# Performance work log

Measured on AMD Instinct MI355X. Metric: run time of the kernel, lower is better.

## Reference

```python
import jax, jax.numpy as jnp
import numpy as np

N_NODES = 100_000
N_EDGES_RAND = 800_000
N_GRAPHS = 2048
IN_FEATS = 74        # CanonicalAtomFeaturizer size
HEADS = 4            # dgllife GAT default num_heads
OUT_FEATS = 32       # dgllife GAT default hidden_feats=[32,32]
PRED_DIM = 128
NEG_SLOPE = 0.2      # dgllife default alpha


def setup_inputs() -> dict:
    key = jax.random.key(0)
    ks = jax.random.split(key, 16)
    feats = jax.random.normal(ks[0], (N_NODES, IN_FEATS), jnp.float32)
    src_r = jax.random.randint(ks[1], (N_EDGES_RAND,), 0, N_NODES, dtype=jnp.int32)
    dst_r = jax.random.randint(ks[2], (N_EDGES_RAND,), 0, N_NODES, dtype=jnp.int32)
    loops = jnp.arange(N_NODES, dtype=jnp.int32)  # self-loops -> no zero in-degree
    src = jnp.concatenate([src_r, loops])
    dst = jnp.concatenate([dst_r, loops])
    # sorted, every graph non-empty, ~49 nodes per molecule
    graph_ids = ((jnp.arange(N_NODES, dtype=jnp.int64) * N_GRAPHS) // N_NODES).astype(jnp.int32)

    def lin(k, i, o):
        return (jax.random.normal(k, (i, o), jnp.float32) / np.sqrt(i)).astype(jnp.float32)

    HF = HEADS * OUT_FEATS
    return {
        'feats': feats, 'src': src, 'dst': dst, 'graph_ids': graph_ids,
        'fc1_w': lin(ks[3], IN_FEATS, HF),
        'attn_l1': jax.random.normal(ks[4], (HEADS, OUT_FEATS), jnp.float32) * 0.1,
        'attn_r1': jax.random.normal(ks[5], (HEADS, OUT_FEATS), jnp.float32) * 0.1,
        'res1_w': lin(ks[6], IN_FEATS, HF),   # residual proj (in != heads*out)
        'bias1': jnp.zeros((HF,), jnp.float32),
        'fc2_w': lin(ks[7], HF, HF),
        'attn_l2': jax.random.normal(ks[8], (HEADS, OUT_FEATS), jnp.float32) * 0.1,
        'attn_r2': jax.random.normal(ks[9], (HEADS, OUT_FEATS), jnp.float32) * 0.1,
        'bias2': jnp.zeros((HF,), jnp.float32),
        'ww': lin(ks[10], OUT_FEATS, 1),
        'wb': jnp.zeros((1,), jnp.float32),
        'tw': lin(ks[11], 2 * OUT_FEATS, PRED_DIM),
        'tb': jnp.zeros((PRED_DIM,), jnp.float32),
    }


def _gat_conv(h, src, dst, fc_w, attn_l, attn_r, bias, res):
    # h: (N, Din) -> (N, H, F). Faithful to dgl.nn.GATConv (bias=True, residual=True).
    N = h.shape[0]
    feat = (h @ fc_w).reshape(N, HEADS, OUT_FEATS)          # (N,H,F)
    el = jnp.sum(feat * attn_l, axis=-1)                    # (N,H)
    er = jnp.sum(feat * attn_r, axis=-1)                    # (N,H)
    e = jax.nn.leaky_relu(el[src] + er[dst], NEG_SLOPE)     # (E,H)
    # edge softmax over incoming edges of each dst node (numerically stable)
    emax = jax.ops.segment_max(e, dst, num_segments=N)      # (N,H)
    ee = jnp.exp(e - emax[dst])
    denom = jax.ops.segment_sum(ee, dst, num_segments=N)    # (N,H)
    a = ee / denom[dst]                                     # (E,H)
    rst = jax.ops.segment_sum(a[:, :, None] * feat[src], dst, num_segments=N)  # (N,H,F)
    return rst + res + bias.reshape(1, HEADS, OUT_FEATS)


def reference(feats, src, dst, graph_ids, fc1_w, attn_l1, attn_r1, res1_w, bias1,
              fc2_w, attn_l2, attn_r2, bias2, ww, wb, tw, tb):
    N = feats.shape[0]
    # Layer 1: residual needs projection (74 != 128); agg 'flatten' + ELU
    res1 = (feats @ res1_w).reshape(N, HEADS, OUT_FEATS)
    h1 = _gat_conv(feats, src, dst, fc1_w, attn_l1, attn_r1, bias1, res1)
    h1 = jax.nn.elu(h1.reshape(N, HEADS * OUT_FEATS))
    # Layer 2: identity residual (128 == heads*out); agg 'mean', no activation
    res2 = h1.reshape(N, HEADS, OUT_FEATS)
    h2 = _gat_conv(h1, src, dst, fc2_w, attn_l2, attn_r2, bias2, res2)
    node_feats = jnp.mean(h2, axis=1)                       # (N, 32)
    # WeightedSumAndMax readout
    w = jax.nn.sigmoid(node_feats @ ww + wb)                # (N,1)
    h_sum = jax.ops.segment_sum(w * node_feats, graph_ids, num_segments=N_GRAPHS)
    h_max = jax.ops.segment_max(node_feats, graph_ids, num_segments=N_GRAPHS)
    g = jnp.concatenate([h_sum, h_max], axis=-1)            # (B, 64)
    return g @ tw + tb                                      # (B, PRED_DIM)
```

## Files before the change

### kernel.cpp

```cpp
#include <hip/hip_runtime.h>
#include <hip/hip_bf16.h>


#define HEADS 4
#define OUTF 32
#define HF 128
#define IN_FEATS 74
#define PRED_DIM 128
#define NEG_SLOPE 0.2f
#define NEG_INF_ENC 0x007fffffu
#define LOG2E 1.4426950408889634f
#define KP1 48
#define KP2 64

typedef __hip_bfloat16 bf16;
typedef __hip_bfloat162 bf16x2;
typedef __attribute__((ext_vector_type(8))) short bf16x8v;
typedef __attribute__((ext_vector_type(4))) float f32x4v;
typedef __attribute__((ext_vector_type(2))) float f32x2v;

__device__ __forceinline__ unsigned enc_f(float f) {
  unsigned u = __float_as_uint(f);
  return (u & 0x80000000u) ? ~u : (u | 0x80000000u);
}
__device__ __forceinline__ float dec_f(unsigned k) {
  return (k & 0x80000000u) ? __uint_as_float(k & 0x7fffffffu)
                           : __uint_as_float(~k);
}
__device__ __forceinline__ unsigned pack_bf16(float a, float b) {
  bf16x2 h = __float22bfloat162_rn(make_float2(a, b));
  return *(unsigned*)&h;
}
__device__ __forceinline__ float2 unpack_bf16(unsigned u) {
  bf16x2 h = *(bf16x2*)&u;
  return __bfloat1622float2(h);
}
__device__ __forceinline__ float lrelu(float v) {
  return fmaxf(v, NEG_SLOPE * v);
}

__global__ __launch_bounds__(256) void prep_w(
    const float* __restrict__ W1, const float* __restrict__ W2,
    const float* __restrict__ W3, unsigned* __restrict__ WT1,
    unsigned* __restrict__ WT2, unsigned* __restrict__ WT3) {
  int t = blockIdx.x * 256 + threadIdx.x;
  if (t < 128 * KP1) {
    int c = t / KP1, kp = t % KP1;
    int k = kp * 2;
    float a1 = (k < IN_FEATS) ? W1[k * HF + c] : 0.f;
    float b1 = (k + 1 < IN_FEATS) ? W1[(k + 1) * HF + c] : 0.f;
    float a2 = (k < IN_FEATS) ? W2[k * HF + c] : 0.f;
    float b2 = (k + 1 < IN_FEATS) ? W2[(k + 1) * HF + c] : 0.f;
    WT1[t] = pack_bf16(a1, b1);
    WT2[t] = pack_bf16(a2, b2);
  } else {
    int u = t - 128 * KP1;
    if (u < 128 * KP2) {
      int c = u / KP2, kp = u % KP2;
      int k = kp * 2;
      WT3[u] = pack_bf16(W3[k * HF + c], W3[(k + 1) * HF + c]);
    }
  }
}

template <typename XT, int K>
__device__ __forceinline__ void stage_X(const XT* __restrict__ X,
                                        unsigned* Xl, int n0, int k0, int N,
                                        int tid) {
  int n = tid >> 2;
  int kp0 = (tid & 3) * 4;
  int gn = n0 + n;
  uint4 val = make_uint4(0u, 0u, 0u, 0u);
  if (gn < N) {
    if (sizeof(XT) == 4) {
      const float* Xf = (const float*)X;
      unsigned v[4];
#pragma unroll
      for (int j = 0; j < 4; ++j) {
        int k = k0 + (kp0 + j) * 2;
        float2 xv = make_float2(0.f, 0.f);
        if (k < K) xv = *(const float2*)&Xf[(size_t)gn * K + k];
        v[j] = pack_bf16(xv.x, xv.y);
      }
      val = make_uint4(v[0], v[1], v[2], v[3]);
    } else {
      const unsigned* Xu = (const unsigned*)X;
      val = *(const uint4*)&Xu[((size_t)gn * K + k0) / 2 + kp0];
    }
  }
  *(uint4*)&Xl[n * 20 + kp0] = val;
}

template <int KP>
__device__ __forceinline__ void stage_Wpre(const unsigned* __restrict__ WT,
                                           unsigned* Wt, int ks, int tid) {
#pragma unroll
  for (int i = 0; i < 8; ++i) {
    int c = tid & 127;
    int kp = i * 2 + (tid >> 7);
    Wt[c * 20 + kp] = WT[c * KP + ks * 16 + kp];
  }
}

__device__ __forceinline__ void scores_epilogue(
    const f32x4v* acc, const float* __restrict__ attn_l,
    const float* __restrict__ attn_r, float* __restrict__ el,
    float* __restrict__ er, int n0, int w, int q, int cc, int N) {
#pragma unroll
  for (int r = 0; r < 4; ++r) {
    int n = n0 + w * 16 + q * 4 + r;
    float pls[4], prs[4];
#pragma unroll
    for (int h = 0; h < 4; ++h) {
      float pl = acc[2 * h][r] * attn_l[h * 32 + cc] +
                 acc[2 * h + 1][r] * attn_l[h * 32 + 16 + cc];
      float pr = acc[2 * h][r] * attn_r[h * 32 + cc] +
                 acc[2 * h + 1][r] * attn_r[h * 32 + 16 + cc];
#pragma unroll
      for (int off = 1; off < 16; off <<= 1) {
        pl += __shfl_xor(pl, off);
        pr += __shfl_xor(pr, off);
      }
      pls[h] = pl;
      prs[h] = pr;
    }
    if (cc == 0 && n < N) {
#pragma unroll
      for (int h = 0; h < 4; ++h) {
        el[n * HEADS + h] = pls[h] * LOG2E;
        er[n * HEADS + h] = prs[h] * LOG2E;
      }
    }
  }
}

template <int K, int KP, typename XT>
__global__ __launch_bounds__(256) void mfma_gemm(
    const XT* __restrict__ X, const unsigned* __restrict__ WT,
    const float* __restrict__ attn_l, const float* __restrict__ attn_r,
    bf16* __restrict__ out, float* __restrict__ el, float* __restrict__ er,
    int N) {
  __shared__ __align__(16) unsigned Xl[64 * 20];
  __shared__ __align__(16) unsigned Wt[128 * 20];
  const int tid = threadIdx.x;
  const int w = tid >> 6;
  const int lane = tid & 63;
  const int cc = lane & 15;
  const int q = lane >> 4;
  const int n0 = blockIdx.x * 64;

  f32x4v acc[8];
#pragma unroll
  for (int t = 0; t < 8; ++t) acc[t] = f32x4v{0.f, 0.f, 0.f, 0.f};

  constexpr int KSTEPS = (K + 31) / 32;
  for (int ks = 0; ks < KSTEPS; ++ks) {
    int k0 = ks * 32;
    stage_X<XT, K>(X, Xl, n0, k0, N, tid);
    stage_Wpre<KP>(WT, Wt, ks, tid);
    __syncthreads();
    bf16x8v a = *(const bf16x8v*)&Xl[(w * 16 + cc) * 20 + q * 4];
#pragma unroll
    for (int t = 0; t < 8; ++t) {
      bf16x8v b = *(const bf16x8v*)&Wt[(t * 16 + cc) * 20 + q * 4];
      acc[t] = __builtin_amdgcn_mfma_f32_16x16x32_bf16(a, b, acc[t], 0, 0, 0);
    }
    __syncthreads();
  }
#pragma unroll
  for (int r = 0; r < 4; ++r) {
    int n = n0 + w * 16 + q * 4 + r;
    if (n < N) {
#pragma unroll
      for (int t = 0; t < 8; ++t)
        out[(size_t)n * HF + t * 16 + cc] = __float2bfloat16(acc[t][r]);
    }
  }
  scores_epilogue(acc, attn_l, attn_r, el, er, n0, w, q, cc, N);
}

template <int K, int KP>
__global__ __launch_bounds__(256) void mfma_dual(
    const float* __restrict__ X, const unsigned* __restrict__ WT1,
    const unsigned* __restrict__ WT2, const float* __restrict__ attn_l,
    const float* __restrict__ attn_r, bf16* __restrict__ outA,
    bf16* __restrict__ outB, float* __restrict__ el, float* __restrict__ er,
    int N) {
  __shared__ __align__(16) unsigned Xl[64 * 20];
  __shared__ __align__(16) unsigned Wt1[128 * 20];
  __shared__ __align__(16) unsigned Wt2[128 * 20];
  const int tid = threadIdx.x;
  const int w = tid >> 6;
  const int lane = tid & 63;
  const int cc = lane & 15;
  const int q = lane >> 4;
  const int n0 = blockIdx.x * 64;

  f32x4v acc1[8], acc2[8];
#pragma unroll
  for (int t = 0; t < 8; ++t) {
    acc1[t] = f32x4v{0.f, 0.f, 0.f, 0.f};
    acc2[t] = f32x4v{0.f, 0.f, 0.f, 0.f};
  }

  constexpr int KSTEPS = (K + 31) / 32;
  for (int ks = 0; ks < KSTEPS; ++ks) {
    int k0 = ks * 32;
    stage_X<float, K>(X, Xl, n0, k0, N, tid);
    stage_Wpre<KP>(WT1, Wt1, ks, tid);
    stage_Wpre<KP>(WT2, Wt2, ks, tid);
    __syncthreads();
    bf16x8v a = *(const bf16x8v*)&Xl[(w * 16 + cc) * 20 + q * 4];
#pragma unroll
    for (int t = 0; t < 8; ++t) {
      bf16x8v b1 = *(const bf16x8v*)&Wt1[(t * 16 + cc) * 20 + q * 4];
      bf16x8v b2 = *(const bf16x8v*)&Wt2[(t * 16 + cc) * 20 + q * 4];
      acc1[t] = __builtin_amdgcn_mfma_f32_16x16x32_bf16(a, b1, acc1[t], 0, 0, 0);
      acc2[t] = __builtin_amdgcn_mfma_f32_16x16x32_bf16(a, b2, acc2[t], 0, 0, 0);
    }
    __syncthreads();
  }
#pragma unroll
  for (int r = 0; r < 4; ++r) {
    int n = n0 + w * 16 + q * 4 + r;
    if (n < N) {
#pragma unroll
      for (int t = 0; t < 8; ++t) {
        outA[(size_t)n * HF + t * 16 + cc] = __float2bfloat16(acc1[t][r]);
        outB[(size_t)n * HF + t * 16 + cc] = __float2bfloat16(acc2[t][r]);
      }
    }
  }
  scores_epilogue(acc1, attn_l, attn_r, el, er, n0, w, q, cc, N);
}

__global__ __launch_bounds__(256) void hist_kernel(
    const int* __restrict__ dst, int* __restrict__ deg,
    int* __restrict__ rank, float* __restrict__ hsum,
    unsigned* __restrict__ hmax, int E, int g32) {
  int e = blockIdx.x * 256 + threadIdx.x;
  if (e < g32) {
    hsum[e] = 0.f;
    hmax[e] = NEG_INF_ENC;
  }
  if (e < E) rank[e] = atomicAdd(&deg[dst[e]], 1);
}

__global__ __launch_bounds__(256) void scan1_kernel(
    const int* __restrict__ deg, int* __restrict__ row_ptr,
    int* __restrict__ bsum, int N) {
  const int base = blockIdx.x * 2048;
  const int tbase = base + threadIdx.x * 8;
  int vals[8];
  int tsum = 0;
#pragma unroll
  for (int i = 0; i < 8; ++i) {
    int idx = tbase + i;
    vals[i] = (idx < N) ? deg[idx] : 0;
    tsum += vals[i];
  }
  const int lane = threadIdx.x & 63, wv = threadIdx.x >> 6;
  int incl = tsum;
#pragma unroll
  for (int off = 1; off < 64; off <<= 1) {
    int nv = __shfl_up(incl, off);
    if (lane >= off) incl += nv;
  }
  __shared__ int wsum[4];
  if (lane == 63) wsum[wv] = incl;
  __syncthreads();
  int woff = 0;
  for (int w = 0; w < wv; ++w) woff += wsum[w];
  int run = woff + incl - tsum;
#pragma unroll
  for (int i = 0; i < 8; ++i) {
    int idx = tbase + i;
    if (idx < N) row_ptr[idx] = run;
    run += vals[i];
  }
  if (threadIdx.x == 255) bsum[blockIdx.x] = woff + incl;
}

__global__ __launch_bounds__(64) void scan2_kernel(
    const int* __restrict__ bsum, int* __restrict__ bpre, int NB) {
  const int lane = threadIdx.x;
  int running = 0;
  for (int c = 0; c < NB; c += 64) {
    int v = (c + lane < NB) ? bsum[c + lane] : 0;
    int incl = v;
#pragma unroll
    for (int off = 1; off < 64; off <<= 1) {
      int nv = __shfl_up(incl, off);
      if (lane >= off) incl += nv;
    }
    if (c + lane < NB) bpre[c + lane] = running + incl - v;
    running += __shfl(incl, 63);
  }
}

__global__ __launch_bounds__(256) void scan3_kernel(
    int* __restrict__ row_ptr, const int* __restrict__ bpre, int N, int E) {
  int t = blockIdx.x * 256 + threadIdx.x;
  if (t < N) row_ptr[t] += bpre[t >> 11];
  if (t == 0) row_ptr[N] = E;
}

__global__ __launch_bounds__(256) void scatter_kernel(
    const int* __restrict__ src, const int* __restrict__ dst,
    const int* __restrict__ row_ptr, const int* __restrict__ rank,
    int* __restrict__ ssorted, int E) {
  int e = blockIdx.x * 256 + threadIdx.x;
  if (e >= E) return;
  int d = dst[e];
  ssorted[row_ptr[d] + rank[e]] = src[e];
}


#define E8_LOAD(i, e_)                                                      \
  const int s##i = __builtin_amdgcn_readfirstlane(ssorted[e_]);             \
  const float xl##i = el[(unsigned)s##i * HEADS + h];                       \
  const unsigned fu##i = *(const unsigned*)&feat[(unsigned)s##i * HF + c2];
#define E8_LOADC(i, e_)                                                     \
  const int s##i = __builtin_amdgcn_readfirstlane(ssorted[min(e_, re - 1)]);\
  const float xl##i = el[(unsigned)s##i * HEADS + h];                       \
  const unsigned fu##i = *(const unsigned*)&feat[(unsigned)s##i * HF + c2];
#define E8_CALC(i)                                                          \
  {                                                                         \
    float xx = __builtin_amdgcn_exp2f(lrelu(xl##i + ern));                  \
    f32x2v ff;                                                              \
    ff.x = __uint_as_float(fu##i << 16);                                    \
    ff.y = __uint_as_float(fu##i & 0xffff0000u);                            \
    ssum += xx;                                                             \
    axy = __builtin_elementwise_fma(f32x2v{xx, xx}, ff, axy);               \
  }
#define E8_CALC_PRED(i, e_)                                                 \
  {                                                                         \
    float xx = __builtin_amdgcn_exp2f(lrelu(xl##i + ern));                  \
    xx = ((e_) + i < re) ? xx : 0.f;                                        \
    f32x2v ff;                                                              \
    ff.x = __uint_as_float(fu##i << 16);                                    \
    ff.y = __uint_as_float(fu##i & 0xffff0000u);                            \
    ssum += xx;                                                             \
    axy = __builtin_elementwise_fma(f32x2v{xx, xx}, ff, axy);               \
  }

#define AGG_LOOP                                                            \
  f32x2v axy = {0.f, 0.f};                                                  \
  float ssum = 0.f;                                                         \
  const int dg = re - rb;                                                   \
  if (dg <= 8) {                                                            \
    E8_LOADC(0, rb) E8_LOADC(1, rb + 1) E8_LOADC(2, rb + 2)                 \
    E8_LOADC(3, rb + 3) E8_LOADC(4, rb + 4) E8_LOADC(5, rb + 5)             \
    E8_LOADC(6, rb + 6) E8_LOADC(7, rb + 7)                                 \
    E8_CALC_PRED(0, rb) E8_CALC_PRED(1, rb) E8_CALC_PRED(2, rb)             \
    E8_CALC_PRED(3, rb) E8_CALC_PRED(4, rb) E8_CALC_PRED(5, rb)             \
    E8_CALC_PRED(6, rb) E8_CALC_PRED(7, rb)                                 \
  } else if (dg <= 16) {                                                    \
    E8_LOAD(0, rb) E8_LOAD(1, rb + 1) E8_LOAD(2, rb + 2)                    \
    E8_LOAD(3, rb + 3) E8_LOAD(4, rb + 4) E8_LOAD(5, rb + 5)                \
    E8_LOAD(6, rb + 6) E8_LOAD(7, rb + 7)                                   \
    E8_LOADC(8, rb + 8) E8_LOADC(9, rb + 9) E8_LOADC(10, rb + 10)           \
    E8_LOADC(11, rb + 11) E8_LOADC(12, rb + 12) E8_LOADC(13, rb + 13)       \
    E8_LOADC(14, rb + 14) E8_LOADC(15, rb + 15)                             \
    E8_CALC(0) E8_CALC(1) E8_CALC(2) E8_CALC(3)                             \
    E8_CALC(4) E8_CALC(5) E8_CALC(6) E8_CALC(7)                             \
    E8_CALC_PRED(8, rb) E8_CALC_PRED(9, rb) E8_CALC_PRED(10, rb)            \
    E8_CALC_PRED(11, rb) E8_CALC_PRED(12, rb) E8_CALC_PRED(13, rb)          \
    E8_CALC_PRED(14, rb) E8_CALC_PRED(15, rb)                               \
  } else {                                                                  \
    int e = rb;                                                             \
    for (; e + 8 <= re; e += 8) {                                           \
      E8_LOAD(0, e) E8_LOAD(1, e + 1) E8_LOAD(2, e + 2) E8_LOAD(3, e + 3)   \
      E8_LOAD(4, e + 4) E8_LOAD(5, e + 5) E8_LOAD(6, e + 6)                 \
      E8_LOAD(7, e + 7)                                                     \
      E8_CALC(0) E8_CALC(1) E8_CALC(2) E8_CALC(3)                           \
      E8_CALC(4) E8_CALC(5) E8_CALC(6) E8_CALC(7)                           \
    }                                                                       \
    if (e < re) {                                                           \
      E8_LOADC(0, e) E8_LOADC(1, e + 1) E8_LOADC(2, e + 2)                  \
      E8_LOADC(3, e + 3) E8_LOADC(4, e + 4) E8_LOADC(5, e + 5)              \
      E8_LOADC(6, e + 6) E8_LOADC(7, e + 7)                                 \
      E8_CALC_PRED(0, e) E8_CALC_PRED(1, e) E8_CALC_PRED(2, e)              \
      E8_CALC_PRED(3, e) E8_CALC_PRED(4, e) E8_CALC_PRED(5, e)              \
      E8_CALC_PRED(6, e) E8_CALC_PRED(7, e)                                 \
    }                                                                       \
  }                                                                         \
  float ax = axy.x, ay = axy.y;

__global__ __launch_bounds__(256) void agg1_fused(
    const int* __restrict__ row_ptr, const int* __restrict__ ssorted,
    const float* __restrict__ el, const float* __restrict__ er,
    const bf16* __restrict__ feat, const bf16* __restrict__ res,
    bf16* __restrict__ H, const float* __restrict__ bias, int N) {
  int n = blockIdx.x * 4 + (threadIdx.x >> 6);
  if (n >= N) return;
  const int lane = threadIdx.x & 63;
  const int c2 = lane * 2, h = lane >> 4;
  const int rb = __builtin_amdgcn_readfirstlane(row_ptr[n]);
  const int re = __builtin_amdgcn_readfirstlane(row_ptr[n + 1]);
  const float ern = er[(unsigned)n * HEADS + h];

  AGG_LOOP

  float inv = 1.f / ssum;
  float2 r = unpack_bf16(*(const unsigned*)&res[(unsigned)n * HF + c2]);
  float2 bi = *(const float2*)&bias[c2];
  float vx = fmaf(ax, inv, r.x + bi.x);
  float vy = fmaf(ay, inv, r.y + bi.y);
  vx = (vx > 0.f) ? vx : expm1f(vx);
  vy = (vy > 0.f) ? vy : expm1f(vy);
  *(unsigned*)&H[(unsigned)n * HF + c2] = pack_bf16(vx, vy);
}

__global__ __launch_bounds__(256) void agg2_fused(
    const int* __restrict__ row_ptr, const int* __restrict__ ssorted,
    const float* __restrict__ el, const float* __restrict__ er,
    const bf16* __restrict__ feat, const bf16* __restrict__ h1,
    const float* __restrict__ bias, const float* __restrict__ ww,
    const float* __restrict__ wb, const int* __restrict__ gids,
    float* __restrict__ hsum, unsigned* __restrict__ hmax, int N) {
  int n = blockIdx.x * 4 + (threadIdx.x >> 6);
  if (n >= N) return;
  const int lane = threadIdx.x & 63;
  const int c2 = lane * 2, h = lane >> 4;
  const int rb = __builtin_amdgcn_readfirstlane(row_ptr[n]);
  const int re = __builtin_amdgcn_readfirstlane(row_ptr[n + 1]);
  const float ern = er[(unsigned)n * HEADS + h];

  AGG_LOOP

  float inv = 1.f / ssum;
  float2 r = unpack_bf16(*(const unsigned*)&h1[(unsigned)n * HF + c2]);
  float2 bi = *(const float2*)&bias[c2];
  ax = fmaf(ax, inv, r.x + bi.x);
  ay = fmaf(ay, inv, r.y + bi.y);
#pragma unroll
  for (int off = 16; off < 64; off <<= 1) {
    ax += __shfl_xor(ax, off);
    ay += __shfl_xor(ay, off);
  }
  ax *= 0.25f;
  ay *= 0.25f;
  int c = c2 & 31;
  float d = fmaf(ax, ww[c], ay * ww[c + 1]);
#pragma unroll
  for (int off = 1; off < 16; off <<= 1) d += __shfl_xor(d, off);
  float wv = 1.f / (1.f + __expf(-(d + wb[0])));
  if (lane < 16) {
    int g = gids[n];
    atomicAdd(&hsum[g * OUTF + c], wv * ax);
    atomicAdd(&hsum[g * OUTF + c + 1], wv * ay);
    atomicMax(&hmax[g * OUTF + c], enc_f(ax));
    atomicMax(&hmax[g * OUTF + c + 1], enc_f(ay));
  }
}

__global__ __launch_bounds__(256) void final_gemm_kernel(
    const float* __restrict__ hsum, const unsigned* __restrict__ hmax,
    const float* __restrict__ tw, const float* __restrict__ tb,
    float* __restrict__ out, int G) {
  __shared__ float tws[64 * PRED_DIM];
  for (int i = threadIdx.x; i < 64 * PRED_DIM; i += 256) tws[i] = tw[i];
  __syncthreads();
  int g = blockIdx.x * 2 + (threadIdx.x >> 7);
  int p = threadIdx.x & 127;
  if (g >= G) return;
  float acc = tb[p];
#pragma unroll
  for (int k = 0; k < OUTF; ++k)
    acc = fmaf(hsum[g * OUTF + k], tws[k * PRED_DIM + p], acc);
#pragma unroll
  for (int k = 0; k < OUTF; ++k)
    acc = fmaf(dec_f(hmax[g * OUTF + k]), tws[(OUTF + k) * PRED_DIM + p], acc);
  out[(size_t)g * PRED_DIM + p] = acc;
}

static inline int cdiv(long long a, int b) { return (int)((a + b - 1) / b); }

extern "C" void kernel_launch(void* const* d_in, const int* in_sizes, int n_in,
                              void* d_out, int out_size, void* d_ws,
                              size_t ws_size, hipStream_t stream) {
  const float* feats   = (const float*)d_in[0];
  const int*   src     = (const int*)d_in[1];
  const int*   dst     = (const int*)d_in[2];
  const int*   gids    = (const int*)d_in[3];
  const float* fc1_w   = (const float*)d_in[4];
  const float* attn_l1 = (const float*)d_in[5];
  const float* attn_r1 = (const float*)d_in[6];
  const float* res1_w  = (const float*)d_in[7];
  const float* bias1   = (const float*)d_in[8];
  const float* fc2_w   = (const float*)d_in[9];
  const float* attn_l2 = (const float*)d_in[10];
  const float* attn_r2 = (const float*)d_in[11];
  const float* bias2   = (const float*)d_in[12];
  const float* ww      = (const float*)d_in[13];
  const float* wb      = (const float*)d_in[14];
  const float* tw      = (const float*)d_in[15];
  const float* tb      = (const float*)d_in[16];
  float* out = (float*)d_out;

  const int N = in_sizes[0] / IN_FEATS;
  const int E = in_sizes[1];
  const int G = out_size / PRED_DIM;
  const int NB = cdiv(N, 2048);

  bf16* A = (bf16*)d_ws;
  bf16* B = A + (size_t)N * HF;
  bf16* H = B + (size_t)N * HF;
  float* el = (float*)(H + (size_t)N * HF);
  float* er = el + (size_t)N * HEADS;
  float* hsum = er + (size_t)N * HEADS;
  unsigned* hmax = (unsigned*)(hsum + (size_t)G * OUTF);
  int* deg     = (int*)(hmax + (size_t)G * OUTF);
  int* row_ptr = deg + N;
  int* ssorted = row_ptr + (N + 1);
  int* rank    = ssorted + E;
  int* bsum    = rank + E;
  int* bpre    = bsum + NB;
  unsigned* WT1 = (unsigned*)(bpre + NB);
  unsigned* WT2 = WT1 + 128 * KP1;
  unsigned* WT3 = WT2 + 128 * KP1;

  const int gblk = cdiv(N, 64);
  const int nwblk = cdiv(N, 4);

  hipMemsetAsync(deg, 0, (size_t)N * sizeof(int), stream);
  prep_w<<<cdiv(128 * (KP1 + KP2), 256), 256, 0, stream>>>(
      fc1_w, res1_w, fc2_w, WT1, WT2, WT3);
  hist_kernel<<<cdiv(E, 256), 256, 0, stream>>>(dst, deg, rank, hsum, hmax, E,
                                                G * OUTF);
  scan1_kernel<<<NB, 256, 0, stream>>>(deg, row_ptr, bsum, N);
  scan2_kernel<<<1, 64, 0, stream>>>(bsum, bpre, NB);
  scan3_kernel<<<cdiv(N, 256), 256, 0, stream>>>(row_ptr, bpre, N, E);
  scatter_kernel<<<cdiv(E, 256), 256, 0, stream>>>(src, dst, row_ptr, rank,
                                                   ssorted, E);

  mfma_dual<IN_FEATS, KP1><<<gblk, 256, 0, stream>>>(
      feats, WT1, WT2, attn_l1, attn_r1, A, B, el, er, N);
  agg1_fused<<<nwblk, 256, 0, stream>>>(row_ptr, ssorted, el, er, A, B, H,
                                        bias1, N);

  mfma_gemm<HF, KP2, bf16><<<gblk, 256, 0, stream>>>(
      H, WT3, attn_l2, attn_r2, A, el, er, N);
  agg2_fused<<<nwblk, 256, 0, stream>>>(row_ptr, ssorted, el, er, A, H, bias2,
                                        ww, wb, gids, hsum, hmax, N);

  final_gemm_kernel<<<cdiv(G, 2), 256, 0, stream>>>(hsum, hmax, tw, tb, out, G);
}
```

Baseline: 367.0 us.

## Precompute per-edge attention exponentials in CSR order before aggregation

```diff
diff --git a/kernel.cpp b/kernel.cpp
--- a/kernel.cpp
+++ b/kernel.cpp
@@ -42,8 +42,10 @@
 __global__ __launch_bounds__(256) void prep_w(
     const float* __restrict__ W1, const float* __restrict__ W2,
     const float* __restrict__ W3, unsigned* __restrict__ WT1,
-    unsigned* __restrict__ WT2, unsigned* __restrict__ WT3) {
+    unsigned* __restrict__ WT2, unsigned* __restrict__ WT3,
+    int* __restrict__ deg, int N) {
   int t = blockIdx.x * 256 + threadIdx.x;
+  if (t < N) deg[t] = 0;
   if (t < 128 * KP1) {
     int c = t / KP1, kp = t % KP1;
     int k = kp * 2;
@@ -305,38 +307,48 @@
   if (t == 0) row_ptr[N] = E;
 }
 
-__global__ __launch_bounds__(256) void scatter_kernel(
+template <bool WRITE_SS>
+__global__ __launch_bounds__(256) void edge_x(
     const int* __restrict__ src, const int* __restrict__ dst,
     const int* __restrict__ row_ptr, const int* __restrict__ rank,
-    int* __restrict__ ssorted, int E) {
+    const float* __restrict__ el, const float* __restrict__ er,
+    int* __restrict__ ssorted, float* __restrict__ xe, int E) {
   int e = blockIdx.x * 256 + threadIdx.x;
   if (e >= E) return;
-  int d = dst[e];
-  ssorted[row_ptr[d] + rank[e]] = src[e];
+  int s = src[e], d = dst[e];
+  int slot = row_ptr[d] + rank[e];
+  if (WRITE_SS) ssorted[slot] = s;
+  float4 l = *(const float4*)&el[(size_t)s * HEADS];
+  float4 r = *(const float4*)&er[(size_t)d * HEADS];
+  float4 o;
+  o.x = __builtin_amdgcn_exp2f(lrelu(l.x + r.x));
+  o.y = __builtin_amdgcn_exp2f(lrelu(l.y + r.y));
+  o.z = __builtin_amdgcn_exp2f(lrelu(l.z + r.z));
+  o.w = __builtin_amdgcn_exp2f(lrelu(l.w + r.w));
+  *(float4*)&xe[(size_t)slot * HEADS] = o;
 }
 
 
 #define E8_LOAD(i, e_)                                                      \
   const int s##i = __builtin_amdgcn_readfirstlane(ssorted[e_]);             \
-  const float xl##i = el[(unsigned)s##i * HEADS + h];                       \
+  const float xv##i = xe[(unsigned)(e_) * HEADS + h];                       \
   const unsigned fu##i = *(const unsigned*)&feat[(unsigned)s##i * HF + c2];
 #define E8_LOADC(i, e_)                                                     \
-  const int s##i = __builtin_amdgcn_readfirstlane(ssorted[min(e_, re - 1)]);\
-  const float xl##i = el[(unsigned)s##i * HEADS + h];                       \
+  const int ec##i = min(e_, re - 1);                                        \
+  const int s##i = __builtin_amdgcn_readfirstlane(ssorted[ec##i]);          \
+  const float xv##i = xe[(unsigned)ec##i * HEADS + h];                      \
   const unsigned fu##i = *(const unsigned*)&feat[(unsigned)s##i * HF + c2];
 #define E8_CALC(i)                                                          \
   {                                                                         \
-    float xx = __builtin_amdgcn_exp2f(lrelu(xl##i + ern));                  \
     f32x2v ff;                                                              \
     ff.x = __uint_as_float(fu##i << 16);                                    \
     ff.y = __uint_as_float(fu##i & 0xffff0000u);                            \
-    ssum += xx;                                                             \
-    axy = __builtin_elementwise_fma(f32x2v{xx, xx}, ff, axy);               \
+    ssum += xv##i;                                                          \
+    axy = __builtin_elementwise_fma(f32x2v{xv##i, xv##i}, ff, axy);         \
   }
 #define E8_CALC_PRED(i, e_)                                                 \
   {                                                                         \
-    float xx = __builtin_amdgcn_exp2f(lrelu(xl##i + ern));                  \
-    xx = ((e_) + i < re) ? xx : 0.f;                                        \
+    float xx = ((e_) + i < re) ? xv##i : 0.f;                               \
     f32x2v ff;                                                              \
     ff.x = __uint_as_float(fu##i << 16);                                    \
     ff.y = __uint_as_float(fu##i & 0xffff0000u);                            \
@@ -389,16 +401,15 @@
 
 __global__ __launch_bounds__(256) void agg1_fused(
     const int* __restrict__ row_ptr, const int* __restrict__ ssorted,
-    const float* __restrict__ el, const float* __restrict__ er,
-    const bf16* __restrict__ feat, const bf16* __restrict__ res,
-    bf16* __restrict__ H, const float* __restrict__ bias, int N) {
+    const float* __restrict__ xe, const bf16* __restrict__ feat,
+    const bf16* __restrict__ res, bf16* __restrict__ H,
+    const float* __restrict__ bias, int N) {
   int n = blockIdx.x * 4 + (threadIdx.x >> 6);
   if (n >= N) return;
   const int lane = threadIdx.x & 63;
   const int c2 = lane * 2, h = lane >> 4;
   const int rb = __builtin_amdgcn_readfirstlane(row_ptr[n]);
   const int re = __builtin_amdgcn_readfirstlane(row_ptr[n + 1]);
-  const float ern = er[(unsigned)n * HEADS + h];
 
   AGG_LOOP
 
@@ -414,18 +425,17 @@
 
 __global__ __launch_bounds__(256) void agg2_fused(
     const int* __restrict__ row_ptr, const int* __restrict__ ssorted,
-    const float* __restrict__ el, const float* __restrict__ er,
-    const bf16* __restrict__ feat, const bf16* __restrict__ h1,
-    const float* __restrict__ bias, const float* __restrict__ ww,
-    const float* __restrict__ wb, const int* __restrict__ gids,
-    float* __restrict__ hsum, unsigned* __restrict__ hmax, int N) {
+    const float* __restrict__ xe, const bf16* __restrict__ feat,
+    const bf16* __restrict__ h1, const float* __restrict__ bias,
+    const float* __restrict__ ww, const float* __restrict__ wb,
+    const int* __restrict__ gids, float* __restrict__ hsum,
+    unsigned* __restrict__ hmax, int N) {
   int n = blockIdx.x * 4 + (threadIdx.x >> 6);
   if (n >= N) return;
   const int lane = threadIdx.x & 63;
   const int c2 = lane * 2, h = lane >> 4;
   const int rb = __builtin_amdgcn_readfirstlane(row_ptr[n]);
   const int re = __builtin_amdgcn_readfirstlane(row_ptr[n + 1]);
-  const float ern = er[(unsigned)n * HEADS + h];
 
   AGG_LOOP
 
@@ -509,7 +519,8 @@
   bf16* H = B + (size_t)N * HF;
   float* el = (float*)(H + (size_t)N * HF);
   float* er = el + (size_t)N * HEADS;
-  float* hsum = er + (size_t)N * HEADS;
+  float* xe = er + (size_t)N * HEADS;
+  float* hsum = xe + (size_t)E * HEADS;
   unsigned* hmax = (unsigned*)(hsum + (size_t)G * OUTF);
   int* deg     = (int*)(hmax + (size_t)G * OUTF);
   int* row_ptr = deg + N;
@@ -523,26 +534,28 @@
 
   const int gblk = cdiv(N, 64);
   const int nwblk = cdiv(N, 4);
-
-  hipMemsetAsync(deg, 0, (size_t)N * sizeof(int), stream);
-  prep_w<<<cdiv(128 * (KP1 + KP2), 256), 256, 0, stream>>>(
-      fc1_w, res1_w, fc2_w, WT1, WT2, WT3);
-  hist_kernel<<<cdiv(E, 256), 256, 0, stream>>>(dst, deg, rank, hsum, hmax, E,
-                                                G * OUTF);
+  const int eblk = cdiv(E, 256);
+
+  prep_w<<<cdiv(N, 256), 256, 0, stream>>>(fc1_w, res1_w, fc2_w, WT1, WT2,
+                                           WT3, deg, N);
+  hist_kernel<<<eblk, 256, 0, stream>>>(dst, deg, rank, hsum, hmax, E,
+                                        G * OUTF);
   scan1_kernel<<<NB, 256, 0, stream>>>(deg, row_ptr, bsum, N);
   scan2_kernel<<<1, 64, 0, stream>>>(bsum, bpre, NB);
   scan3_kernel<<<cdiv(N, 256), 256, 0, stream>>>(row_ptr, bpre, N, E);
-  scatter_kernel<<<cdiv(E, 256), 256, 0, stream>>>(src, dst, row_ptr, rank,
-                                                   ssorted, E);
 
   mfma_dual<IN_FEATS, KP1><<<gblk, 256, 0, stream>>>(
       feats, WT1, WT2, attn_l1, attn_r1, A, B, el, er, N);
-  agg1_fused<<<nwblk, 256, 0, stream>>>(row_ptr, ssorted, el, er, A, B, H,
-                                        bias1, N);
+  edge_x<true><<<eblk, 256, 0, stream>>>(src, dst, row_ptr, rank, el, er,
+                                         ssorted, xe, E);
+  agg1_fused<<<nwblk, 256, 0, stream>>>(row_ptr, ssorted, xe, A, B, H, bias1,
+                                        N);
 
   mfma_gemm<HF, KP2, bf16><<<gblk, 256, 0, stream>>>(
       H, WT3, attn_l2, attn_r2, A, el, er, N);
-  agg2_fused<<<nwblk, 256, 0, stream>>>(row_ptr, ssorted, el, er, A, H, bias2,
+  edge_x<false><<<eblk, 256, 0, stream>>>(src, dst, row_ptr, rank, el, er,
+                                          ssorted, xe, E);
+  agg2_fused<<<nwblk, 256, 0, stream>>>(row_ptr, ssorted, xe, A, H, bias2,
                                         ww, wb, gids, hsum, hmax, N);
 
   final_gemm_kernel<<<cdiv(G, 2), 256, 0, stream>>>(hsum, hmax, tw, tb, out, G);
```

Measured after the change: 417.3 us. 13.7% more time.

## Load MFMA operands directly from global memory, fold memset, pad edge list

Applied to the files above, without the earlier changes.

```diff
diff --git a/kernel.cpp b/kernel.cpp
--- a/kernel.cpp
+++ b/kernel.cpp
@@ -42,8 +42,10 @@
 __global__ __launch_bounds__(256) void prep_w(
     const float* __restrict__ W1, const float* __restrict__ W2,
     const float* __restrict__ W3, unsigned* __restrict__ WT1,
-    unsigned* __restrict__ WT2, unsigned* __restrict__ WT3) {
+    unsigned* __restrict__ WT2, unsigned* __restrict__ WT3,
+    int* __restrict__ deg, int N) {
   int t = blockIdx.x * 256 + threadIdx.x;
+  if (t < N) deg[t] = 0;
   if (t < 128 * KP1) {
     int c = t / KP1, kp = t % KP1;
     int k = kp * 2;
@@ -63,43 +65,28 @@
   }
 }
 
-template <typename XT, int K>
-__device__ __forceinline__ void stage_X(const XT* __restrict__ X,
-                                        unsigned* Xl, int n0, int k0, int N,
-                                        int tid) {
-  int n = tid >> 2;
-  int kp0 = (tid & 3) * 4;
-  int gn = n0 + n;
-  uint4 val = make_uint4(0u, 0u, 0u, 0u);
-  if (gn < N) {
-    if (sizeof(XT) == 4) {
-      const float* Xf = (const float*)X;
-      unsigned v[4];
-#pragma unroll
-      for (int j = 0; j < 4; ++j) {
-        int k = k0 + (kp0 + j) * 2;
-        float2 xv = make_float2(0.f, 0.f);
-        if (k < K) xv = *(const float2*)&Xf[(size_t)gn * K + k];
-        v[j] = pack_bf16(xv.x, xv.y);
+
+template <int K>
+__device__ __forceinline__ bf16x8v load_a_f32(const float* __restrict__ X,
+                                              int row, int N, int ks, int q) {
+  unsigned v[4] = {0u, 0u, 0u, 0u};
+  if (row < N) {
+    const float* base = X + (size_t)row * K;
+    int k = ks * 32 + q * 8;
+#pragma unroll
+    for (int j = 0; j < 4; ++j) {
+      int kk = k + j * 2;
+      if (kk + 1 < K) {
+        float2 f = *(const float2*)&base[kk];
+        v[j] = pack_bf16(f.x, f.y);
+      } else if (kk < K) {
+        v[j] = pack_bf16(base[kk], 0.f);
       }
-      val = make_uint4(v[0], v[1], v[2], v[3]);
-    } else {
-      const unsigned* Xu = (const unsigned*)X;
-      val = *(const uint4*)&Xu[((size_t)gn * K + k0) / 2 + kp0];
-    }
-  }
-  *(uint4*)&Xl[n * 20 + kp0] = val;
-}
-
-template <int KP>
-__device__ __forceinline__ void stage_Wpre(const unsigned* __restrict__ WT,
-                                           unsigned* Wt, int ks, int tid) {
-#pragma unroll
-  for (int i = 0; i < 8; ++i) {
-    int c = tid & 127;
-    int kp = i * 2 + (tid >> 7);
-    Wt[c * 20 + kp] = WT[c * KP + ks * 16 + kp];
-  }
+    }
+  }
+  union { unsigned u[4]; bf16x8v v8; } r;
+  r.u[0] = v[0]; r.u[1] = v[1]; r.u[2] = v[2]; r.u[3] = v[3];
+  return r.v8;
 }
 
 __device__ __forceinline__ void scores_epilogue(
@@ -134,38 +121,33 @@
   }
 }
 
-template <int K, int KP, typename XT>
+template <int K, int KP>
 __global__ __launch_bounds__(256) void mfma_gemm(
-    const XT* __restrict__ X, const unsigned* __restrict__ WT,
+    const bf16* __restrict__ X, const unsigned* __restrict__ WT,
     const float* __restrict__ attn_l, const float* __restrict__ attn_r,
     bf16* __restrict__ out, float* __restrict__ el, float* __restrict__ er,
     int N) {
-  __shared__ __align__(16) unsigned Xl[64 * 20];
-  __shared__ __align__(16) unsigned Wt[128 * 20];
   const int tid = threadIdx.x;
   const int w = tid >> 6;
   const int lane = tid & 63;
   const int cc = lane & 15;
   const int q = lane >> 4;
   const int n0 = blockIdx.x * 64;
+  const int arow = n0 + w * 16 + cc;
 
   f32x4v acc[8];
 #pragma unroll
   for (int t = 0; t < 8; ++t) acc[t] = f32x4v{0.f, 0.f, 0.f, 0.f};
 
   constexpr int KSTEPS = (K + 31) / 32;
+#pragma unroll
   for (int ks = 0; ks < KSTEPS; ++ks) {
-    int k0 = ks * 32;
-    stage_X<XT, K>(X, Xl, n0, k0, N, tid);
-    stage_Wpre<KP>(WT, Wt, ks, tid);
-    __syncthreads();
-    bf16x8v a = *(const bf16x8v*)&Xl[(w * 16 + cc) * 20 + q * 4];
+    bf16x8v a = *(const bf16x8v*)&X[(size_t)arow * K + ks * 32 + q * 8];
 #pragma unroll
     for (int t = 0; t < 8; ++t) {
-      bf16x8v b = *(const bf16x8v*)&Wt[(t * 16 + cc) * 20 + q * 4];
+      bf16x8v b = *(const bf16x8v*)&WT[(t * 16 + cc) * KP + ks * 16 + q * 4];
       acc[t] = __builtin_amdgcn_mfma_f32_16x16x32_bf16(a, b, acc[t], 0, 0, 0);
     }
-    __syncthreads();
   }
 #pragma unroll
   for (int r = 0; r < 4; ++r) {
@@ -186,15 +168,13 @@
     const float* __restrict__ attn_r, bf16* __restrict__ outA,
     bf16* __restrict__ outB, float* __restrict__ el, float* __restrict__ er,
     int N) {
-  __shared__ __align__(16) unsigned Xl[64 * 20];
-  __shared__ __align__(16) unsigned Wt1[128 * 20];
-  __shared__ __align__(16) unsigned Wt2[128 * 20];
   const int tid = threadIdx.x;
   const int w = tid >> 6;
   const int lane = tid & 63;
   const int cc = lane & 15;
   const int q = lane >> 4;
   const int n0 = blockIdx.x * 64;
+  const int arow = n0 + w * 16 + cc;
 
   f32x4v acc1[8], acc2[8];
 #pragma unroll
@@ -204,21 +184,16 @@
   }
 
   constexpr int KSTEPS = (K + 31) / 32;
+#pragma unroll
   for (int ks = 0; ks < KSTEPS; ++ks) {
-    int k0 = ks * 32;
-    stage_X<float, K>(X, Xl, n0, k0, N, tid);
-    stage_Wpre<KP>(WT1, Wt1, ks, tid);
-    stage_Wpre<KP>(WT2, Wt2, ks, tid);
-    __syncthreads();
-    bf16x8v a = *(const bf16x8v*)&Xl[(w * 16 + cc) * 20 + q * 4];
+    bf16x8v a = load_a_f32<K>(X, arow, N, ks, q);
 #pragma unroll
     for (int t = 0; t < 8; ++t) {
-      bf16x8v b1 = *(const bf16x8v*)&Wt1[(t * 16 + cc) * 20 + q * 4];
-      bf16x8v b2 = *(const bf16x8v*)&Wt2[(t * 16 + cc) * 20 + q * 4];
+      bf16x8v b1 = *(const bf16x8v*)&WT1[(t * 16 + cc) * KP + ks * 16 + q * 4];
+      bf16x8v b2 = *(const bf16x8v*)&WT2[(t * 16 + cc) * KP + ks * 16 + q * 4];
       acc1[t] = __builtin_amdgcn_mfma_f32_16x16x32_bf16(a, b1, acc1[t], 0, 0, 0);
       acc2[t] = __builtin_amdgcn_mfma_f32_16x16x32_bf16(a, b2, acc2[t], 0, 0, 0);
     }
-    __syncthreads();
   }
 #pragma unroll
   for (int r = 0; r < 4; ++r) {
@@ -311,6 +286,7 @@
     int* __restrict__ ssorted, int E) {
   int e = blockIdx.x * 256 + threadIdx.x;
   if (e >= E) return;
+  if (e < 16) ssorted[E + e] = 0;
   int d = dst[e];
   ssorted[row_ptr[d] + rank[e]] = src[e];
 }
@@ -318,10 +294,6 @@
 
 #define E8_LOAD(i, e_)                                                      \
   const int s##i = __builtin_amdgcn_readfirstlane(ssorted[e_]);             \
-  const float xl##i = el[(unsigned)s##i * HEADS + h];                       \
-  const unsigned fu##i = *(const unsigned*)&feat[(unsigned)s##i * HF + c2];
-#define E8_LOADC(i, e_)                                                     \
-  const int s##i = __builtin_amdgcn_readfirstlane(ssorted[min(e_, re - 1)]);\
   const float xl##i = el[(unsigned)s##i * HEADS + h];                       \
   const unsigned fu##i = *(const unsigned*)&feat[(unsigned)s##i * HF + c2];
 #define E8_CALC(i)                                                          \
@@ -349,9 +321,9 @@
   float ssum = 0.f;                                                         \
   const int dg = re - rb;                                                   \
   if (dg <= 8) {                                                            \
-    E8_LOADC(0, rb) E8_LOADC(1, rb + 1) E8_LOADC(2, rb + 2)                 \
-    E8_LOADC(3, rb + 3) E8_LOADC(4, rb + 4) E8_LOADC(5, rb + 5)             \
-    E8_LOADC(6, rb + 6) E8_LOADC(7, rb + 7)                                 \
+    E8_LOAD(0, rb) E8_LOAD(1, rb + 1) E8_LOAD(2, rb + 2)                    \
+    E8_LOAD(3, rb + 3) E8_LOAD(4, rb + 4) E8_LOAD(5, rb + 5)                \
+    E8_LOAD(6, rb + 6) E8_LOAD(7, rb + 7)                                   \
     E8_CALC_PRED(0, rb) E8_CALC_PRED(1, rb) E8_CALC_PRED(2, rb)             \
     E8_CALC_PRED(3, rb) E8_CALC_PRED(4, rb) E8_CALC_PRED(5, rb)             \
     E8_CALC_PRED(6, rb) E8_CALC_PRED(7, rb)                                 \
@@ -359,9 +331,9 @@
     E8_LOAD(0, rb) E8_LOAD(1, rb + 1) E8_LOAD(2, rb + 2)                    \
     E8_LOAD(3, rb + 3) E8_LOAD(4, rb + 4) E8_LOAD(5, rb + 5)                \
     E8_LOAD(6, rb + 6) E8_LOAD(7, rb + 7)                                   \
-    E8_LOADC(8, rb + 8) E8_LOADC(9, rb + 9) E8_LOADC(10, rb + 10)           \
-    E8_LOADC(11, rb + 11) E8_LOADC(12, rb + 12) E8_LOADC(13, rb + 13)       \
-    E8_LOADC(14, rb + 14) E8_LOADC(15, rb + 15)                             \
+    E8_LOAD(8, rb + 8) E8_LOAD(9, rb + 9) E8_LOAD(10, rb + 10)              \
+    E8_LOAD(11, rb + 11) E8_LOAD(12, rb + 12) E8_LOAD(13, rb + 13)          \
+    E8_LOAD(14, rb + 14) E8_LOAD(15, rb + 15)                               \
     E8_CALC(0) E8_CALC(1) E8_CALC(2) E8_CALC(3)                             \
     E8_CALC(4) E8_CALC(5) E8_CALC(6) E8_CALC(7)                             \
     E8_CALC_PRED(8, rb) E8_CALC_PRED(9, rb) E8_CALC_PRED(10, rb)            \
@@ -377,9 +349,9 @@
       E8_CALC(4) E8_CALC(5) E8_CALC(6) E8_CALC(7)                           \
     }                                                                       \
     if (e < re) {                                                           \
-      E8_LOADC(0, e) E8_LOADC(1, e + 1) E8_LOADC(2, e + 2)                  \
-      E8_LOADC(3, e + 3) E8_LOADC(4, e + 4) E8_LOADC(5, e + 5)              \
-      E8_LOADC(6, e + 6) E8_LOADC(7, e + 7)                                 \
+      E8_LOAD(0, e) E8_LOAD(1, e + 1) E8_LOAD(2, e + 2) E8_LOAD(3, e + 3)   \
+      E8_LOAD(4, e + 4) E8_LOAD(5, e + 5) E8_LOAD(6, e + 6)                 \
+      E8_LOAD(7, e + 7)                                                     \
       E8_CALC_PRED(0, e) E8_CALC_PRED(1, e) E8_CALC_PRED(2, e)              \
       E8_CALC_PRED(3, e) E8_CALC_PRED(4, e) E8_CALC_PRED(5, e)              \
       E8_CALC_PRED(6, e) E8_CALC_PRED(7, e)                                 \
@@ -514,19 +486,19 @@
   int* deg     = (int*)(hmax + (size_t)G * OUTF);
   int* row_ptr = deg + N;
   int* ssorted = row_ptr + (N + 1);
-  int* rank    = ssorted + E;
+  int* rank    = ssorted + E + 16;
   int* bsum    = rank + E;
   int* bpre    = bsum + NB;
-  unsigned* WT1 = (unsigned*)(bpre + NB);
+  unsigned* WT1 = (unsigned*)(((uintptr_t)(bpre + NB) + 15) &
+                              ~(uintptr_t)15);
   unsigned* WT2 = WT1 + 128 * KP1;
   unsigned* WT3 = WT2 + 128 * KP1;
 
   const int gblk = cdiv(N, 64);
   const int nwblk = cdiv(N, 4);
 
-  hipMemsetAsync(deg, 0, (size_t)N * sizeof(int), stream);
-  prep_w<<<cdiv(128 * (KP1 + KP2), 256), 256, 0, stream>>>(
-      fc1_w, res1_w, fc2_w, WT1, WT2, WT3);
+  prep_w<<<cdiv(N, 256), 256, 0, stream>>>(fc1_w, res1_w, fc2_w, WT1, WT2,
+                                           WT3, deg, N);
   hist_kernel<<<cdiv(E, 256), 256, 0, stream>>>(dst, deg, rank, hsum, hmax, E,
                                                 G * OUTF);
   scan1_kernel<<<NB, 256, 0, stream>>>(deg, row_ptr, bsum, N);
@@ -540,7 +512,7 @@
   agg1_fused<<<nwblk, 256, 0, stream>>>(row_ptr, ssorted, el, er, A, B, H,
                                         bias1, N);
 
-  mfma_gemm<HF, KP2, bf16><<<gblk, 256, 0, stream>>>(
+  mfma_gemm<HF, KP2><<<gblk, 256, 0, stream>>>(
       H, WT3, attn_l2, attn_r2, A, el, er, N);
   agg2_fused<<<nwblk, 256, 0, stream>>>(row_ptr, ssorted, el, er, A, H, bias2,
                                         ww, wb, gids, hsum, hmax, N);
```

New measurement: 350.0 us. 4.6% less time.
